# Kernel optimization log

Measured on AMD Instinct MI355X. Metric: run time of the kernel, lower is better.

## Reference

```python
import jax, jax.numpy as jnp
import numpy as np

B, T, D = 2, 2048, 1024
H, HD = 16, 64
DL, DC = 512, 256
THETA = 10000.0
LN_EPS = 1e-5


def setup_inputs() -> dict:
    key = jax.random.key(0)
    ks = jax.random.split(key, 8)
    s = 0.02
    return {
        "x": jax.random.normal(ks[0], (B, T, D), jnp.float32),
        "W_q": jax.random.normal(ks[1], (H * HD, D), jnp.float32) * s,
        "b_q": jnp.zeros((H * HD,), jnp.float32),
        "W_kvl": jax.random.normal(ks[2], (DL, D), jnp.float32) * s,
        "b_kvl": jnp.zeros((DL,), jnp.float32),
        "ts_scale": jnp.ones((DL,), jnp.float32),
        "ts_shift": jnp.zeros((DL,), jnp.float32),
        "W_comp": jax.random.normal(ks[3], (DC, DL), jnp.float32) * s,
        "W_exp": jax.random.normal(ks[4], (DL, DC), jnp.float32) * s,
        "ln_g": jnp.ones((DC,), jnp.float32),
        "ln_b": jnp.zeros((DC,), jnp.float32),
        "W_fkv": jax.random.normal(ks[5], (2 * H * HD, DL), jnp.float32) * s,
        "b_fkv": jnp.zeros((2 * H * HD,), jnp.float32),
        "W_out": jax.random.normal(ks[6], (D, H * HD), jnp.float32) * s,
        "b_out": jnp.zeros((D,), jnp.float32),
    }


def _rope_tables(t_len):
    inv_freq = 1.0 / (THETA ** (jnp.arange(0, HD, 2, dtype=jnp.float32) / HD))
    pos = jnp.arange(t_len, dtype=jnp.float32)
    freqs = pos[:, None] * inv_freq[None, :]          # [T, HD/2]
    cos = jnp.concatenate([jnp.cos(freqs)] * 2, -1)   # [T, HD]
    sin = jnp.concatenate([jnp.sin(freqs)] * 2, -1)
    return cos[None, None], sin[None, None]           # [1,1,T,HD]


def _rotate_half(z):
    return jnp.concatenate([-z[..., HD // 2:], z[..., :HD // 2]], -1)


def reference(x, W_q, b_q, W_kvl, b_kvl, ts_scale, ts_shift, W_comp, W_exp,
              ln_g, ln_b, W_fkv, b_fkv, W_out, b_out):
    # Q path: [B,T,D] -> [B,H,T,HD]
    q = (jnp.einsum('btd,ed->bte', x, W_q) + b_q).reshape(B, T, H, HD).transpose(0, 2, 1, 3)

    # KV latent + learned KVSplice bottleneck
    kvl = jnp.einsum('btd,ld->btl', x, W_kvl) + b_kvl                 # [B,T,DL]
    xt = kvl * jax.nn.softplus(ts_scale) + ts_shift
    c = jnp.einsum('btl,cl->btc', xt, W_comp)                         # [B,T,DC]
    mu = jnp.mean(c, -1, keepdims=True)
    var = jnp.mean(jnp.square(c - mu), -1, keepdims=True)
    c = (c - mu) * jax.lax.rsqrt(var + LN_EPS) * ln_g + ln_b
    dec = jnp.einsum('btc,lc->btl', c, W_exp)                         # [B,T,DL]

    # Decompress latent to K,V
    kv = jnp.einsum('btl,el->bte', dec, W_fkv) + b_fkv                # [B,T,2*H*HD]
    kv = kv.reshape(B, T, 2, H, HD).transpose(2, 0, 3, 1, 4)          # [2,B,H,T,HD]
    k, v = kv[0], kv[1]

    # RoPE
    cos, sin = _rope_tables(T)
    q = q * cos + _rotate_half(q) * sin
    k = k * cos + _rotate_half(k) * sin

    # Causal SDPA
    scale = 1.0 / np.sqrt(HD)
    scores = jnp.einsum('bhqd,bhkd->bhqk', q, k) * scale
    mask = jnp.tril(jnp.ones((T, T), bool))
    scores = jnp.where(mask, scores, jnp.float32(-1e30))
    attn = jax.nn.softmax(scores, axis=-1)
    o = jnp.einsum('bhqk,bhkd->bhqd', attn, v)
    o = o.transpose(0, 2, 1, 3).reshape(B, T, H * HD)
    return jnp.einsum('bte,de->btd', o, W_out) + b_out
```

## Files before the change

kernel.cpp:

```cpp
#include <hip/hip_runtime.h>
#include <math.h>

#define B_SZ   2
#define T_SEQ  2048
#define NH     16
#define HDIM   64
#define D_MOD  1024
#define DL     512
#define DC     256
#define MROWS  4096

typedef __attribute__((ext_vector_type(8))) short bf16x8;
typedef __attribute__((ext_vector_type(4))) float f32x4;

#define SCALE_Q 0.18033688011112042f

static __device__ __forceinline__ unsigned short f2bf(float f) {
    union { float f; unsigned u; } v; v.f = f;
    unsigned r = v.u + 0x7fffu + ((v.u >> 16) & 1u);
    return (unsigned short)(r >> 16);
}

static __device__ __forceinline__ void gl_lds16(const unsigned short* g,
                                                unsigned short* l) {
    __builtin_amdgcn_global_load_lds(
        (const __attribute__((address_space(1))) unsigned int*)g,
        (__attribute__((address_space(3))) unsigned int*)l, 16, 0, 0);
}

__global__ __launch_bounds__(256) void cvt_bf16(
    const float* __restrict__ x,  const float* __restrict__ wq,
    const float* __restrict__ wkvl, const float* __restrict__ wcomp,
    const float* __restrict__ wexp, const float* __restrict__ wfkv,
    const float* __restrict__ wout,
    unsigned short* __restrict__ xb,  unsigned short* __restrict__ wqh,
    unsigned short* __restrict__ wkvlh, unsigned short* __restrict__ wcomph,
    unsigned short* __restrict__ wexph, unsigned short* __restrict__ wfkvh,
    unsigned short* __restrict__ wouth, float2* __restrict__ rope_tab)
{
    const int g = blockIdx.x * 256 + threadIdx.x;
    const int stride = gridDim.x * 256;
#define CVT_SEG(src, dst, n4)                                              \
    for (int i = g; i < (n4); i += stride) {                               \
        float4 v = ((const float4*)(src))[i];                              \
        unsigned short h[4] = {f2bf(v.x), f2bf(v.y), f2bf(v.z), f2bf(v.w)};\
        *(uint2*)((dst) + (size_t)i * 4) = *(uint2*)h;                     \
    }
    CVT_SEG(x, xb, 1048576)
    CVT_SEG(wq, wqh, 262144)
    CVT_SEG(wkvl, wkvlh, 131072)
    CVT_SEG(wcomp, wcomph, 32768)
    CVT_SEG(wexp, wexph, 32768)
    CVT_SEG(wfkv, wfkvh, 262144)
    CVT_SEG(wout, wouth, 262144)
#undef CVT_SEG
    for (int i = g; i < T_SEQ * 32; i += stride) {
        const int t = i >> 5, fi = i & 31;
        const float inv = __expf((float)fi * (-9.210340371976184f / 32.0f));
        float sn, cs; sincosf((float)t * inv, &sn, &cs);
        rope_tab[i] = make_float2(cs, sn);
    }
}

#define GEMM64R_PROLOG(Aptr, Wptr, Kdim)                                       \
    __shared__ unsigned short As[64 * 64];                                     \
    __shared__ unsigned short Ws[64 * 64];                                     \
    const int tid = threadIdx.x;                                               \
    const int w = tid >> 6, lane = tid & 63;                                   \
    const int l16 = lane & 15, quad = lane >> 4;                               \
    const int sw8 = ((lane & 7) ^ ((lane >> 3) & 7)) << 3;                     \
    const int srow = lane >> 3;                                                \
    const unsigned short* Ag0 = (Aptr) + (size_t)(m0 + w * 16 + srow) * (Kdim) + sw8;      \
    const unsigned short* Ag1 = (Aptr) + (size_t)(m0 + w * 16 + 8 + srow) * (Kdim) + sw8;  \
    const unsigned short* Wg0 = (Wptr) + (size_t)(n0 + w * 16 + srow) * (Kdim) + sw8;      \
    const unsigned short* Wg1 = (Wptr) + (size_t)(n0 + w * 16 + 8 + srow) * (Kdim) + sw8;  \
    unsigned short* Al0 = &As[(w * 16) * 64];                                  \
    unsigned short* Al1 = &As[(w * 16 + 8) * 64];                              \
    unsigned short* Wl0 = &Ws[(w * 16) * 64];                                  \
    unsigned short* Wl1 = &Ws[(w * 16 + 8) * 64];                              \
    const int xh = (l16 & 7);                                                  \
    f32x4 acc[4];                                                              \
    _Pragma("unroll") for (int j = 0; j < 4; ++j)                              \
        acc[j] = (f32x4){0.f, 0.f, 0.f, 0.f};                                  \
    for (int k0 = 0; k0 < (Kdim); k0 += 64) {                                  \
        __syncthreads();                                                       \
        gl_lds16(Ag0 + k0, Al0);                                               \
        gl_lds16(Ag1 + k0, Al1);                                               \
        gl_lds16(Wg0 + k0, Wl0);                                               \
        gl_lds16(Wg1 + k0, Wl1);                                               \
        __syncthreads();                                                       \
        bf16x8 af[2], bfr[4][2];                                               \
        _Pragma("unroll") for (int kk = 0; kk < 2; ++kk)                       \
            af[kk] = *(const bf16x8*)&As[(w * 16 + l16) * 64 +                 \
                                         (((kk * 4 + quad) ^ xh) << 3)];       \
        _Pragma("unroll") for (int j = 0; j < 4; ++j)                          \
            _Pragma("unroll") for (int kk = 0; kk < 2; ++kk)                   \
                bfr[j][kk] = *(const bf16x8*)&Ws[(j * 16 + l16) * 64 +         \
                                             (((kk * 4 + quad) ^ xh) << 3)];   \
        _Pragma("unroll") for (int kk = 0; kk < 2; ++kk)                       \
            _Pragma("unroll") for (int j = 0; j < 4; ++j)                      \
                acc[j] = __builtin_amdgcn_mfma_f32_16x16x32_bf16(              \
                    af[kk], bfr[j][kk], acc[j], 0, 0, 0);                      \
    }

__global__ __launch_bounds__(256) void gemm_qxt(
    const unsigned short* __restrict__ A, const unsigned short* __restrict__ Wq,
    const unsigned short* __restrict__ Wkvl,
    const float* __restrict__ b_q, const float* __restrict__ b_kvl,
    const float* __restrict__ ts_scale, const float* __restrict__ ts_shift,
    const float2* __restrict__ tab,
    unsigned short* __restrict__ qh, unsigned short* __restrict__ xt)
{
    const int m0 = blockIdx.x * 64;
    const bool is_q = (blockIdx.y < 16);
    const int n0 = is_q ? blockIdx.y * 64 : (blockIdx.y - 16) * 64;
    const unsigned short* W = is_q ? Wq : Wkvl;

    GEMM64R_PROLOG(A, W, D_MOD)

    if (is_q) {
#pragma unroll
        for (int j = 0; j < 4; ++j) {
            const int col = n0 + j * 16 + l16;
            const int h = col >> 6, hd = col & 63;
            const float bv = b_q[col];
            const float bvp = b_q[col ^ 32];
            const float sgn = (hd < 32) ? -1.f : 1.f;
#pragma unroll
            for (int reg = 0; reg < 4; ++reg) {
                const int row = m0 + w * 16 + quad * 4 + reg;
                const int b = row >> 11, t = row & (T_SEQ - 1);
                const float2 cssn = tab[t * 32 + (hd & 31)];
                const float v  = acc[j][reg] + bv;
                const float vp = acc[j ^ 2][reg] + bvp;
                const float r = (v * cssn.x + sgn * vp * cssn.y) * SCALE_Q;
                qh[(((size_t)b * NH + h) * T_SEQ + t) * HDIM + hd] = f2bf(r);
            }
        }
    } else {
#pragma unroll
        for (int j = 0; j < 4; ++j) {
            const int col = n0 + j * 16 + l16;
            const float bv = b_kvl[col];
            const float sp_s = log1pf(expf(ts_scale[col]));
            const float sp_t = ts_shift[col];
#pragma unroll
            for (int reg = 0; reg < 4; ++reg) {
                const int row = m0 + w * 16 + quad * 4 + reg;
                const float val = (acc[j][reg] + bv) * sp_s + sp_t;
                xt[(size_t)row * DL + col] = f2bf(val);
            }
        }
    }
}

__global__ __launch_bounds__(256) void gemm_kv(
    const unsigned short* __restrict__ A, const unsigned short* __restrict__ W,
    const float* __restrict__ bias, const float2* __restrict__ tab,
    unsigned short* __restrict__ kh, unsigned short* __restrict__ vth)
{
    const int m0 = blockIdx.x * 64, n0 = blockIdx.y * 64;

    GEMM64R_PROLOG(A, W, DL)

    if (n0 < 1024) {
#pragma unroll
        for (int j = 0; j < 4; ++j) {
            const int col = n0 + j * 16 + l16;
            const int h = (col >> 6) & 15, hd = col & 63;
            const float bv = bias[col];
            const float bvp = bias[col ^ 32];
            const float sgn = (hd < 32) ? -1.f : 1.f;
#pragma unroll
            for (int reg = 0; reg < 4; ++reg) {
                const int row = m0 + w * 16 + quad * 4 + reg;
                const int b = row >> 11, t = row & (T_SEQ - 1);
                const float2 cssn = tab[t * 32 + (hd & 31)];
                const float v  = acc[j][reg] + bv;
                const float vp = acc[j ^ 2][reg] + bvp;
                const float r = v * cssn.x + sgn * vp * cssn.y;
                kh[(((size_t)b * NH + h) * T_SEQ + t) * HDIM + hd] = f2bf(r);
            }
        }
    } else {
#pragma unroll
        for (int j = 0; j < 4; ++j) {
            const int col = n0 + j * 16 + l16;
            const int cv = col - 1024;
            const int h = cv >> 6, hd = cv & 63;
            const float bv = bias[col];
            unsigned short hv[4];
            const int r0 = m0 + w * 16 + quad * 4;
            const int b = r0 >> 11, t0 = r0 & (T_SEQ - 1);
#pragma unroll
            for (int reg = 0; reg < 4; ++reg)
                hv[reg] = f2bf(acc[j][reg] + bv);
            *(uint2*)&vth[(((size_t)b * NH + h) * HDIM + hd) * T_SEQ + t0] =
                *(uint2*)hv;
        }
    }
}

__global__ __launch_bounds__(256) void gemm_out(
    const unsigned short* __restrict__ A, const unsigned short* __restrict__ W,
    const float* __restrict__ bias, float* __restrict__ C)
{
    const int m0 = blockIdx.x * 64, n0 = blockIdx.y * 64;

    GEMM64R_PROLOG(A, W, D_MOD)

#pragma unroll
    for (int j = 0; j < 4; ++j) {
        const int col = n0 + j * 16 + l16;
        const float bv = bias[col];
#pragma unroll
        for (int reg = 0; reg < 4; ++reg) {
            const int row = m0 + w * 16 + quad * 4 + reg;
            C[(size_t)row * D_MOD + col] = acc[j][reg] + bv;
        }
    }
}

__global__ __launch_bounds__(256) void gemm_b(
    const unsigned short* __restrict__ A, const unsigned short* __restrict__ W,
    unsigned short* __restrict__ dec)
{
    const int m0 = blockIdx.x * 64, n0 = blockIdx.y * 64;

    GEMM64R_PROLOG(A, W, DC)

#pragma unroll
    for (int j = 0; j < 4; ++j) {
        const int col = n0 + j * 16 + l16;
#pragma unroll
        for (int reg = 0; reg < 4; ++reg) {
            const int row = m0 + w * 16 + quad * 4 + reg;
            dec[(size_t)row * DL + col] = f2bf(acc[j][reg]);
        }
    }
}

__global__ __launch_bounds__(256) void gemm_c_ln(
    const unsigned short* __restrict__ A, const unsigned short* __restrict__ W,
    const float* __restrict__ g, const float* __restrict__ bta,
    unsigned short* __restrict__ outb)
{
    __shared__ unsigned short As[16 * 32];
    __shared__ unsigned short Ws[256 * 32];
    __shared__ float redS[4][16];
    __shared__ float redQ[4][16];

    const int tid = threadIdx.x;
    const int w = tid >> 6, lane = tid & 63;
    const int l16 = lane & 15, quad = lane >> 4;
    const int m0 = blockIdx.x * 16;

    const int srow = lane >> 2, scol = (lane & 3) << 3;
    const unsigned short* Ag = A + (size_t)(m0 + srow) * DL + scol;
    const unsigned short* Wg = W + (size_t)(w * 64 + srow) * DL + scol;

    f32x4 acc[4];
#pragma unroll
    for (int j = 0; j < 4; ++j) acc[j] = (f32x4){0.f, 0.f, 0.f, 0.f};

    for (int k0 = 0; k0 < DL; k0 += 32) {
        __syncthreads();
        if (w == 0) gl_lds16(Ag + k0, &As[0]);
#pragma unroll
        for (int c = 0; c < 4; ++c)
            gl_lds16(Wg + (size_t)(c * 16) * DL + k0, &Ws[(w * 64 + c * 16) * 32]);
        __syncthreads();

        const bf16x8 af = *(const bf16x8*)&As[l16 * 32 + quad * 8];
        bf16x8 bfr[4];
#pragma unroll
        for (int j = 0; j < 4; ++j)
            bfr[j] = *(const bf16x8*)&Ws[(w * 64 + j * 16 + l16) * 32 + quad * 8];
#pragma unroll
        for (int j = 0; j < 4; ++j)
            acc[j] = __builtin_amdgcn_mfma_f32_16x16x32_bf16(af, bfr[j], acc[j], 0, 0, 0);
    }

    float s[4], q2[4];
#pragma unroll
    for (int reg = 0; reg < 4; ++reg) {
        float sv = (acc[0][reg] + acc[1][reg]) + (acc[2][reg] + acc[3][reg]);
        float qv = (acc[0][reg] * acc[0][reg] + acc[1][reg] * acc[1][reg]) +
                   (acc[2][reg] * acc[2][reg] + acc[3][reg] * acc[3][reg]);
#pragma unroll
        for (int off = 1; off < 16; off <<= 1) {
            sv += __shfl_xor(sv, off);
            qv += __shfl_xor(qv, off);
        }
        s[reg] = sv; q2[reg] = qv;
    }
    if (l16 == 0) {
#pragma unroll
        for (int reg = 0; reg < 4; ++reg) {
            redS[w][quad * 4 + reg] = s[reg];
            redQ[w][quad * 4 + reg] = q2[reg];
        }
    }
    __syncthreads();

#pragma unroll
    for (int reg = 0; reg < 4; ++reg) {
        const int r = quad * 4 + reg;
        const float sum = (redS[0][r] + redS[1][r]) + (redS[2][r] + redS[3][r]);
        const float sq  = (redQ[0][r] + redQ[1][r]) + (redQ[2][r] + redQ[3][r]);
        const float mu  = sum * (1.0f / DC);
        const float var = sq * (1.0f / DC) - mu * mu;
        const float rstd = rsqrtf(var + 1e-5f);
#pragma unroll
        for (int j = 0; j < 4; ++j) {
            const int col = w * 64 + j * 16 + l16;
            const float val = (acc[j][reg] - mu) * rstd * g[col] + bta[col];
            outb[(size_t)(m0 + r) * DC + col] = f2bf(val);
        }
    }
}

__global__ __launch_bounds__(256, 3) void flash_mfma(
    const unsigned short* __restrict__ q, const unsigned short* __restrict__ k,
    const unsigned short* __restrict__ vt, unsigned short* __restrict__ o)
{
    __shared__ unsigned short Ks[64 * 72];
    __shared__ unsigned short Vs[64 * 72];
    __shared__ unsigned short Ps[64 * 72];

    const int bh = blockIdx.x & 31;
    const int j  = 31 - (blockIdx.x >> 5);
    const int q0 = j * 64;
    const int tid = threadIdx.x;
    const int w = tid >> 6, lane = tid & 63;
    const int l16 = lane & 15, quad = lane >> 4;
    const int rbase = q0 + w * 16;

    bf16x8 qf[2];
#pragma unroll
    for (int kk = 0; kk < 2; ++kk)
        qf[kk] = *(const bf16x8*)(q + ((size_t)bh * T_SEQ + rbase + l16) * HDIM + kk * 32 + quad * 8);

    f32x4 of[4];
    float lrow[4];
#pragma unroll
    for (int dt = 0; dt < 4; ++dt) of[dt] = (f32x4){0.f, 0.f, 0.f, 0.f};
#pragma unroll
    for (int r = 0; r < 4; ++r) lrow[r] = 0.f;

    const int ldr = tid >> 2;
    const int ldc = (tid & 3) * 16;
    const unsigned short* kgb = k + ((size_t)bh * T_SEQ + ldr) * HDIM + ldc;
    const unsigned short* vgb = vt + ((size_t)bh * HDIM + ldr) * T_SEQ + ldc;

    const int kend = (j + 1) * 64;
    for (int k0 = 0; k0 < kend; k0 += 64) {
        __syncthreads();
        {
            const unsigned short* kg = kgb + (size_t)k0 * HDIM;
            *(bf16x8*)&Ks[ldr * 72 + ldc]     = *(const bf16x8*)kg;
            *(bf16x8*)&Ks[ldr * 72 + ldc + 8] = *(const bf16x8*)(kg + 8);
            const unsigned short* vg = vgb + k0;
            *(bf16x8*)&Vs[ldr * 72 + ldc]     = *(const bf16x8*)vg;
            *(bf16x8*)&Vs[ldr * 72 + ldc + 8] = *(const bf16x8*)(vg + 8);
        }
        __syncthreads();

        bf16x8 kf[4][2];
#pragma unroll
        for (int nt = 0; nt < 4; ++nt)
#pragma unroll
            for (int kk = 0; kk < 2; ++kk)
                kf[nt][kk] = *(const bf16x8*)&Ks[(nt * 16 + l16) * 72 + kk * 32 + quad * 8];

        f32x4 sf[4];
#pragma unroll
        for (int nt = 0; nt < 4; ++nt) {
            sf[nt] = (f32x4){0.f, 0.f, 0.f, 0.f};
#pragma unroll
            for (int kk = 0; kk < 2; ++kk)
                sf[nt] = __builtin_amdgcn_mfma_f32_16x16x32_bf16(qf[kk], kf[nt][kk], sf[nt], 0, 0, 0);
        }

        const bool need_mask = (k0 + 63) > rbase;
#pragma unroll
        for (int reg = 0; reg < 4; ++reg) {
            float a0 = sf[0][reg], a1 = sf[1][reg], a2 = sf[2][reg], a3 = sf[3][reg];
            if (need_mask) {
                const int tq = rbase + quad * 4 + reg;
                if (k0 +      l16 > tq) a0 = -1e30f;
                if (k0 + 16 + l16 > tq) a1 = -1e30f;
                if (k0 + 32 + l16 > tq) a2 = -1e30f;
                if (k0 + 48 + l16 > tq) a3 = -1e30f;
            }
            union { float f; unsigned u; } u0, u1, u2, u3;
            u0.f = exp2f(a0); u1.f = exp2f(a1);
            u2.f = exp2f(a2); u3.f = exp2f(a3);
            const int prow = (w * 16 + quad * 4 + reg) * 72 + l16;
            Ps[prow]      = (unsigned short)(u0.u >> 16);
            Ps[prow + 16] = (unsigned short)(u1.u >> 16);
            Ps[prow + 32] = (unsigned short)(u2.u >> 16);
            Ps[prow + 48] = (unsigned short)(u3.u >> 16);
            u0.u &= 0xffff0000u; u1.u &= 0xffff0000u;
            u2.u &= 0xffff0000u; u3.u &= 0xffff0000u;
            lrow[reg] += (u0.f + u1.f) + (u2.f + u3.f);
        }

        bf16x8 vf[4][2];
#pragma unroll
        for (int dt = 0; dt < 4; ++dt)
#pragma unroll
            for (int kk = 0; kk < 2; ++kk)
                vf[dt][kk] = *(const bf16x8*)&Vs[(dt * 16 + l16) * 72 + kk * 32 + quad * 8];

        bf16x8 pf[2];
#pragma unroll
        for (int kk = 0; kk < 2; ++kk)
            pf[kk] = *(const bf16x8*)&Ps[(w * 16 + l16) * 72 + kk * 32 + quad * 8];
#pragma unroll
        for (int dt = 0; dt < 4; ++dt)
#pragma unroll
            for (int kk = 0; kk < 2; ++kk)
                of[dt] = __builtin_amdgcn_mfma_f32_16x16x32_bf16(pf[kk], vf[dt][kk], of[dt], 0, 0, 0);
    }

    const int b = bh >> 4, h = bh & 15;
#pragma unroll
    for (int reg = 0; reg < 4; ++reg) {
        float l = lrow[reg];
        l += __shfl_xor(l, 1);
        l += __shfl_xor(l, 2);
        l += __shfl_xor(l, 4);
        l += __shfl_xor(l, 8);
        const float inv = 1.0f / l;
        const int t = rbase + quad * 4 + reg;
#pragma unroll
        for (int dt = 0; dt < 4; ++dt)
            o[((size_t)b * T_SEQ + t) * (NH * HDIM) + h * HDIM + dt * 16 + l16] =
                f2bf(of[dt][reg] * inv);
    }
}

extern "C" void kernel_launch(void* const* d_in, const int* in_sizes, int n_in,
                              void* d_out, int out_size, void* d_ws, size_t ws_size,
                              hipStream_t stream)
{
    (void)in_sizes; (void)n_in; (void)out_size; (void)ws_size;

    const float* x        = (const float*)d_in[0];
    const float* W_q      = (const float*)d_in[1];
    const float* b_q      = (const float*)d_in[2];
    const float* W_kvl    = (const float*)d_in[3];
    const float* b_kvl    = (const float*)d_in[4];
    const float* ts_scale = (const float*)d_in[5];
    const float* ts_shift = (const float*)d_in[6];
    const float* W_comp   = (const float*)d_in[7];
    const float* W_exp    = (const float*)d_in[8];
    const float* ln_g     = (const float*)d_in[9];
    const float* ln_b     = (const float*)d_in[10];
    const float* W_fkv    = (const float*)d_in[11];
    const float* b_fkv    = (const float*)d_in[12];
    const float* W_out    = (const float*)d_in[13];
    const float* b_out    = (const float*)d_in[14];
    float* out = (float*)d_out;

    char* p = (char*)d_ws;
    unsigned short* xb     = (unsigned short*)p;             p += 8  * 1024 * 1024;
    unsigned short* wqh    = (unsigned short*)p;             p += 2  * 1024 * 1024;
    unsigned short* wkvlh  = (unsigned short*)p;             p += 1  * 1024 * 1024;
    unsigned short* wcomph = (unsigned short*)p;             p += 256 * 1024;
    unsigned short* wexph  = (unsigned short*)p;             p += 256 * 1024;
    unsigned short* wfkvh  = (unsigned short*)p;             p += 2  * 1024 * 1024;
    unsigned short* wouth  = (unsigned short*)p;             p += 2  * 1024 * 1024;
    unsigned short* qh     = (unsigned short*)p;             p += 8  * 1024 * 1024;
    unsigned short* kh     = (unsigned short*)p;             p += 8  * 1024 * 1024;
    unsigned short* vth    = (unsigned short*)p;             p += 8  * 1024 * 1024;
    unsigned short* xt     = (unsigned short*)p;             p += 4  * 1024 * 1024;
    unsigned short* cbh    = (unsigned short*)p;             p += 2  * 1024 * 1024;
    unsigned short* dec    = (unsigned short*)p;             p += 4  * 1024 * 1024;
    unsigned short* ob     = (unsigned short*)p;             p += 8  * 1024 * 1024;
    float2*         tab    = (float2*)p;                     p += 512 * 1024;

    const dim3 blk(256);

    cvt_bf16<<<1024, blk, 0, stream>>>(x, W_q, W_kvl, W_comp, W_exp, W_fkv, W_out,
                                       xb, wqh, wkvlh, wcomph, wexph, wfkvh, wouth,
                                       tab);

    gemm_qxt<<<dim3(64, 24), blk, 0, stream>>>(
        xb, wqh, wkvlh, b_q, b_kvl, ts_scale, ts_shift, tab, qh, xt);

    gemm_c_ln<<<256, blk, 0, stream>>>(
        xt, wcomph, ln_g, ln_b, cbh);

    gemm_b<<<dim3(64, 8), blk, 0, stream>>>(
        cbh, wexph, dec);

    gemm_kv<<<dim3(64, 32), blk, 0, stream>>>(
        dec, wfkvh, b_fkv, tab, kh, vth);

    flash_mfma<<<1024, blk, 0, stream>>>(qh, kh, vth, ob);

    gemm_out<<<dim3(64, 16), blk, 0, stream>>>(
        ob, wouth, b_out, out);
}
```

Before: 223.1 us.

## Use 128x128 block tiles with 2x2 warp layout for large GEMMs

Replaces the 64x64 block-tile GEMM core used by the Q/latent, K/V and output projections with a 128x128 tile in which each of four waves computes a 64x64 sub-tile (4x4 MFMA accumulators). Each LDS fragment load is now reused across four MFMAs instead of fewer, which raises arithmetic intensity and cuts global and LDS traffic per flop. The trade-off is a quarter as many blocks (e.g. 256–512 per launch on a 256-CU part), higher register use (64 accumulator floats per lane) and possibly lower occupancy or tail imbalance.

```diff
diff --git a/kernel.cpp b/kernel.cpp
--- a/kernel.cpp
+++ b/kernel.cpp
@@ -59,6 +59,179 @@
         const float inv = __expf((float)fi * (-9.210340371976184f / 32.0f));
         float sn, cs; sincosf((float)t * inv, &sn, &cs);
         rope_tab[i] = make_float2(cs, sn);
+    }
+}
+
+#define GEMM128_PROLOG(Aptr, Wptr, Kdim)                                       \
+    __shared__ unsigned short As[128 * 64];                                    \
+    __shared__ unsigned short Ws[128 * 64];                                    \
+    const int tid = threadIdx.x;                                               \
+    const int w = tid >> 6, lane = tid & 63;                                   \
+    const int l16 = lane & 15, quad = lane >> 4;                               \
+    const int wr = w >> 1, wc = w & 1;                                         \
+    const int srow = lane >> 3;                                                \
+    const int sw8 = ((lane & 7) ^ srow) << 3;                                  \
+    const unsigned short* Ag = (Aptr) + (size_t)(m0 + w * 32 + srow) * (Kdim) + sw8; \
+    const unsigned short* Wg = (Wptr) + (size_t)(n0 + w * 32 + srow) * (Kdim) + sw8; \
+    unsigned short* Al = &As[(w * 32) * 64];                                   \
+    unsigned short* Wl = &Ws[(w * 32) * 64];                                   \
+    const int xh = l16 & 7;                                                    \
+    f32x4 acc[4][4];                                                           \
+    _Pragma("unroll") for (int mi = 0; mi < 4; ++mi)                           \
+        _Pragma("unroll") for (int nj = 0; nj < 4; ++nj)                       \
+            acc[mi][nj] = (f32x4){0.f, 0.f, 0.f, 0.f};                         \
+    for (int k0 = 0; k0 < (Kdim); k0 += 64) {                                  \
+        __syncthreads();                                                       \
+        _Pragma("unroll") for (int seg = 0; seg < 4; ++seg) {                  \
+            gl_lds16(Ag + (size_t)(seg * 8) * (Kdim) + k0, Al + seg * 512);    \
+            gl_lds16(Wg + (size_t)(seg * 8) * (Kdim) + k0, Wl + seg * 512);    \
+        }                                                                      \
+        __syncthreads();                                                       \
+        _Pragma("unroll") for (int kk = 0; kk < 2; ++kk) {                     \
+            bf16x8 af[4], bfr[4];                                              \
+            _Pragma("unroll") for (int mi = 0; mi < 4; ++mi)                   \
+                af[mi] = *(const bf16x8*)&As[(wr * 64 + mi * 16 + l16) * 64 +  \
+                                             (((kk * 4 + quad) ^ xh) << 3)];   \
+            _Pragma("unroll") for (int nj = 0; nj < 4; ++nj)                   \
+                bfr[nj] = *(const bf16x8*)&Ws[(wc * 64 + nj * 16 + l16) * 64 + \
+                                              (((kk * 4 + quad) ^ xh) << 3)];  \
+            _Pragma("unroll") for (int mi = 0; mi < 4; ++mi)                   \
+                _Pragma("unroll") for (int nj = 0; nj < 4; ++nj)               \
+                    acc[mi][nj] = __builtin_amdgcn_mfma_f32_16x16x32_bf16(     \
+                        af[mi], bfr[nj], acc[mi][nj], 0, 0, 0);                \
+        }                                                                      \
+    }
+
+__global__ __launch_bounds__(256) void gemm_qxt(
+    const unsigned short* __restrict__ A, const unsigned short* __restrict__ Wq,
+    const unsigned short* __restrict__ Wkvl,
+    const float* __restrict__ b_q, const float* __restrict__ b_kvl,
+    const float* __restrict__ ts_scale, const float* __restrict__ ts_shift,
+    const float2* __restrict__ tab,
+    unsigned short* __restrict__ qh, unsigned short* __restrict__ xt)
+{
+    const int m0 = blockIdx.x * 128;
+    const bool is_q = (blockIdx.y < 8);
+    const int n0 = is_q ? blockIdx.y * 128 : (blockIdx.y - 8) * 128;
+    const unsigned short* W = is_q ? Wq : Wkvl;
+
+    GEMM128_PROLOG(A, W, D_MOD)
+
+    if (is_q) {
+#pragma unroll
+        for (int nj = 0; nj < 4; ++nj) {
+            const int col = n0 + wc * 64 + nj * 16 + l16;
+            const int h = col >> 6, hd = col & 63;
+            const float bv = b_q[col];
+            const float bvp = b_q[col ^ 32];
+            const float sgn = (hd < 32) ? -1.f : 1.f;
+#pragma unroll
+            for (int mi = 0; mi < 4; ++mi) {
+#pragma unroll
+                for (int reg = 0; reg < 4; ++reg) {
+                    const int row = m0 + wr * 64 + mi * 16 + quad * 4 + reg;
+                    const int b = row >> 11, t = row & (T_SEQ - 1);
+                    const float2 cssn = tab[t * 32 + (hd & 31)];
+                    const float v  = acc[mi][nj][reg] + bv;
+                    const float vp = acc[mi][nj ^ 2][reg] + bvp;
+                    const float r = (v * cssn.x + sgn * vp * cssn.y) * SCALE_Q;
+                    qh[(((size_t)b * NH + h) * T_SEQ + t) * HDIM + hd] = f2bf(r);
+                }
+            }
+        }
+    } else {
+#pragma unroll
+        for (int nj = 0; nj < 4; ++nj) {
+            const int col = n0 + wc * 64 + nj * 16 + l16;
+            const float bv = b_kvl[col];
+            const float sp_s = log1pf(expf(ts_scale[col]));
+            const float sp_t = ts_shift[col];
+#pragma unroll
+            for (int mi = 0; mi < 4; ++mi) {
+#pragma unroll
+                for (int reg = 0; reg < 4; ++reg) {
+                    const int row = m0 + wr * 64 + mi * 16 + quad * 4 + reg;
+                    const float val = (acc[mi][nj][reg] + bv) * sp_s + sp_t;
+                    xt[(size_t)row * DL + col] = f2bf(val);
+                }
+            }
+        }
+    }
+}
+
+__global__ __launch_bounds__(256) void gemm_kv(
+    const unsigned short* __restrict__ A, const unsigned short* __restrict__ W,
+    const float* __restrict__ bias, const float2* __restrict__ tab,
+    unsigned short* __restrict__ kh, unsigned short* __restrict__ vth)
+{
+    const int m0 = blockIdx.x * 128, n0 = blockIdx.y * 128;
+
+    GEMM128_PROLOG(A, W, DL)
+
+    if (n0 < 1024) {
+#pragma unroll
+        for (int nj = 0; nj < 4; ++nj) {
+            const int col = n0 + wc * 64 + nj * 16 + l16;
+            const int h = (col >> 6) & 15, hd = col & 63;
+            const float bv = bias[col];
+            const float bvp = bias[col ^ 32];
+            const float sgn = (hd < 32) ? -1.f : 1.f;
+#pragma unroll
+            for (int mi = 0; mi < 4; ++mi) {
+#pragma unroll
+                for (int reg = 0; reg < 4; ++reg) {
+                    const int row = m0 + wr * 64 + mi * 16 + quad * 4 + reg;
+                    const int b = row >> 11, t = row & (T_SEQ - 1);
+                    const float2 cssn = tab[t * 32 + (hd & 31)];
+                    const float v  = acc[mi][nj][reg] + bv;
+                    const float vp = acc[mi][nj ^ 2][reg] + bvp;
+                    const float r = v * cssn.x + sgn * vp * cssn.y;
+                    kh[(((size_t)b * NH + h) * T_SEQ + t) * HDIM + hd] = f2bf(r);
+                }
+            }
+        }
+    } else {
+#pragma unroll
+        for (int nj = 0; nj < 4; ++nj) {
+            const int col = n0 + wc * 64 + nj * 16 + l16;
+            const int cv = col - 1024;
+            const int h = cv >> 6, hd = cv & 63;
+            const float bv = bias[col];
+#pragma unroll
+            for (int mi = 0; mi < 4; ++mi) {
+                unsigned short hv[4];
+                const int r0 = m0 + wr * 64 + mi * 16 + quad * 4;
+                const int b = r0 >> 11, t0 = r0 & (T_SEQ - 1);
+#pragma unroll
+                for (int reg = 0; reg < 4; ++reg)
+                    hv[reg] = f2bf(acc[mi][nj][reg] + bv);
+                *(uint2*)&vth[(((size_t)b * NH + h) * HDIM + hd) * T_SEQ + t0] =
+                    *(uint2*)hv;
+            }
+        }
+    }
+}
+
+__global__ __launch_bounds__(256) void gemm_out(
+    const unsigned short* __restrict__ A, const unsigned short* __restrict__ W,
+    const float* __restrict__ bias, float* __restrict__ C)
+{
+    const int m0 = blockIdx.x * 128, n0 = blockIdx.y * 128;
+
+    GEMM128_PROLOG(A, W, D_MOD)
+
+#pragma unroll
+    for (int nj = 0; nj < 4; ++nj) {
+        const int col = n0 + wc * 64 + nj * 16 + l16;
+        const float bv = bias[col];
+#pragma unroll
+        for (int mi = 0; mi < 4; ++mi) {
+#pragma unroll
+            for (int reg = 0; reg < 4; ++reg) {
+                const int row = m0 + wr * 64 + mi * 16 + quad * 4 + reg;
+                C[(size_t)row * D_MOD + col] = acc[mi][nj][reg] + bv;
+            }
+        }
     }
 }
 
@@ -103,124 +276,6 @@
                     af[kk], bfr[j][kk], acc[j], 0, 0, 0);                      \
     }
 
-__global__ __launch_bounds__(256) void gemm_qxt(
-    const unsigned short* __restrict__ A, const unsigned short* __restrict__ Wq,
-    const unsigned short* __restrict__ Wkvl,
-    const float* __restrict__ b_q, const float* __restrict__ b_kvl,
-    const float* __restrict__ ts_scale, const float* __restrict__ ts_shift,
-    const float2* __restrict__ tab,
-    unsigned short* __restrict__ qh, unsigned short* __restrict__ xt)
-{
-    const int m0 = blockIdx.x * 64;
-    const bool is_q = (blockIdx.y < 16);
-    const int n0 = is_q ? blockIdx.y * 64 : (blockIdx.y - 16) * 64;
-    const unsigned short* W = is_q ? Wq : Wkvl;
-
-    GEMM64R_PROLOG(A, W, D_MOD)
-
-    if (is_q) {
-#pragma unroll
-        for (int j = 0; j < 4; ++j) {
-            const int col = n0 + j * 16 + l16;
-            const int h = col >> 6, hd = col & 63;
-            const float bv = b_q[col];
-            const float bvp = b_q[col ^ 32];
-            const float sgn = (hd < 32) ? -1.f : 1.f;
-#pragma unroll
-            for (int reg = 0; reg < 4; ++reg) {
-                const int row = m0 + w * 16 + quad * 4 + reg;
-                const int b = row >> 11, t = row & (T_SEQ - 1);
-                const float2 cssn = tab[t * 32 + (hd & 31)];
-                const float v  = acc[j][reg] + bv;
-                const float vp = acc[j ^ 2][reg] + bvp;
-                const float r = (v * cssn.x + sgn * vp * cssn.y) * SCALE_Q;
-                qh[(((size_t)b * NH + h) * T_SEQ + t) * HDIM + hd] = f2bf(r);
-            }
-        }
-    } else {
-#pragma unroll
-        for (int j = 0; j < 4; ++j) {
-            const int col = n0 + j * 16 + l16;
-            const float bv = b_kvl[col];
-            const float sp_s = log1pf(expf(ts_scale[col]));
-            const float sp_t = ts_shift[col];
-#pragma unroll
-            for (int reg = 0; reg < 4; ++reg) {
-                const int row = m0 + w * 16 + quad * 4 + reg;
-                const float val = (acc[j][reg] + bv) * sp_s + sp_t;
-                xt[(size_t)row * DL + col] = f2bf(val);
-            }
-        }
-    }
-}
-
-__global__ __launch_bounds__(256) void gemm_kv(
-    const unsigned short* __restrict__ A, const unsigned short* __restrict__ W,
-    const float* __restrict__ bias, const float2* __restrict__ tab,
-    unsigned short* __restrict__ kh, unsigned short* __restrict__ vth)
-{
-    const int m0 = blockIdx.x * 64, n0 = blockIdx.y * 64;
-
-    GEMM64R_PROLOG(A, W, DL)
-
-    if (n0 < 1024) {
-#pragma unroll
-        for (int j = 0; j < 4; ++j) {
-            const int col = n0 + j * 16 + l16;
-            const int h = (col >> 6) & 15, hd = col & 63;
-            const float bv = bias[col];
-            const float bvp = bias[col ^ 32];
-            const float sgn = (hd < 32) ? -1.f : 1.f;
-#pragma unroll
-            for (int reg = 0; reg < 4; ++reg) {
-                const int row = m0 + w * 16 + quad * 4 + reg;
-                const int b = row >> 11, t = row & (T_SEQ - 1);
-                const float2 cssn = tab[t * 32 + (hd & 31)];
-                const float v  = acc[j][reg] + bv;
-                const float vp = acc[j ^ 2][reg] + bvp;
-                const float r = v * cssn.x + sgn * vp * cssn.y;
-                kh[(((size_t)b * NH + h) * T_SEQ + t) * HDIM + hd] = f2bf(r);
-            }
-        }
-    } else {
-#pragma unroll
-        for (int j = 0; j < 4; ++j) {
-            const int col = n0 + j * 16 + l16;
-            const int cv = col - 1024;
-            const int h = cv >> 6, hd = cv & 63;
-            const float bv = bias[col];
-            unsigned short hv[4];
-            const int r0 = m0 + w * 16 + quad * 4;
-            const int b = r0 >> 11, t0 = r0 & (T_SEQ - 1);
-#pragma unroll
-            for (int reg = 0; reg < 4; ++reg)
-                hv[reg] = f2bf(acc[j][reg] + bv);
-            *(uint2*)&vth[(((size_t)b * NH + h) * HDIM + hd) * T_SEQ + t0] =
-                *(uint2*)hv;
-        }
-    }
-}
-
-__global__ __launch_bounds__(256) void gemm_out(
-    const unsigned short* __restrict__ A, const unsigned short* __restrict__ W,
-    const float* __restrict__ bias, float* __restrict__ C)
-{
-    const int m0 = blockIdx.x * 64, n0 = blockIdx.y * 64;
-
-    GEMM64R_PROLOG(A, W, D_MOD)
-
-#pragma unroll
-    for (int j = 0; j < 4; ++j) {
-        const int col = n0 + j * 16 + l16;
-        const float bv = bias[col];
-#pragma unroll
-        for (int reg = 0; reg < 4; ++reg) {
-            const int row = m0 + w * 16 + quad * 4 + reg;
-            C[(size_t)row * D_MOD + col] = acc[j][reg] + bv;
-        }
-    }
-}
-
 __global__ __launch_bounds__(256) void gemm_b(
     const unsigned short* __restrict__ A, const unsigned short* __restrict__ W,
     unsigned short* __restrict__ dec)
@@ -487,7 +542,7 @@
                                        xb, wqh, wkvlh, wcomph, wexph, wfkvh, wouth,
                                        tab);
 
-    gemm_qxt<<<dim3(64, 24), blk, 0, stream>>>(
+    gemm_qxt<<<dim3(32, 12), blk, 0, stream>>>(
         xb, wqh, wkvlh, b_q, b_kvl, ts_scale, ts_shift, tab, qh, xt);
 
     gemm_c_ln<<<256, blk, 0, stream>>>(
@@ -496,11 +551,11 @@
     gemm_b<<<dim3(64, 8), blk, 0, stream>>>(
         cbh, wexph, dec);
 
-    gemm_kv<<<dim3(64, 32), blk, 0, stream>>>(
+    gemm_kv<<<dim3(32, 16), blk, 0, stream>>>(
         dec, wfkvh, b_fkv, tab, kh, vth);
 
     flash_mfma<<<1024, blk, 0, stream>>>(qh, kh, vth, ob);
 
-    gemm_out<<<dim3(64, 16), blk, 0, stream>>>(
+    gemm_out<<<dim3(32, 8), blk, 0, stream>>>(
         ob, wouth, b_out, out);
 }
```

Result: slower. 244.9 us (+9.8%).

## Double-buffer K/V tiles with register prefetch and raise MFMA wave priority

Applied to the files above, without the earlier changes.

The flash attention loop now loads the next K and V tile from global memory into registers while the current tile is being computed. It stores the tiles into two alternating LDS buffers, which removes one of the two barriers per iteration. It also wraps both MFMA blocks in s_setprio so waves issuing matrix instructions get scheduling priority. The cost is double the K/V LDS footprint and extra registers, which could reduce occupancy at the declared launch bounds.

```diff
diff --git a/kernel.cpp b/kernel.cpp
--- a/kernel.cpp
+++ b/kernel.cpp
@@ -324,8 +324,8 @@
     const unsigned short* __restrict__ q, const unsigned short* __restrict__ k,
     const unsigned short* __restrict__ vt, unsigned short* __restrict__ o)
 {
-    __shared__ unsigned short Ks[64 * 72];
-    __shared__ unsigned short Vs[64 * 72];
+    __shared__ unsigned short Ks[2][64 * 72];
+    __shared__ unsigned short Vs[2][64 * 72];
     __shared__ unsigned short Ps[64 * 72];
 
     const int bh = blockIdx.x & 31;
@@ -353,27 +353,37 @@
     const unsigned short* kgb = k + ((size_t)bh * T_SEQ + ldr) * HDIM + ldc;
     const unsigned short* vgb = vt + ((size_t)bh * HDIM + ldr) * T_SEQ + ldc;
 
+    bf16x8 kr0 = *(const bf16x8*)kgb;
+    bf16x8 kr1 = *(const bf16x8*)(kgb + 8);
+    bf16x8 vr0 = *(const bf16x8*)vgb;
+    bf16x8 vr1 = *(const bf16x8*)(vgb + 8);
+
     const int kend = (j + 1) * 64;
-    for (int k0 = 0; k0 < kend; k0 += 64) {
+    int buf = 0;
+    for (int k0 = 0; k0 < kend; k0 += 64, buf ^= 1) {
+        *(bf16x8*)&Ks[buf][ldr * 72 + ldc]     = kr0;
+        *(bf16x8*)&Ks[buf][ldr * 72 + ldc + 8] = kr1;
+        *(bf16x8*)&Vs[buf][ldr * 72 + ldc]     = vr0;
+        *(bf16x8*)&Vs[buf][ldr * 72 + ldc + 8] = vr1;
+        if (k0 + 64 < kend) {
+            const unsigned short* kg = kgb + (size_t)(k0 + 64) * HDIM;
+            const unsigned short* vg = vgb + (k0 + 64);
+            kr0 = *(const bf16x8*)kg;
+            kr1 = *(const bf16x8*)(kg + 8);
+            vr0 = *(const bf16x8*)vg;
+            vr1 = *(const bf16x8*)(vg + 8);
+        }
         __syncthreads();
-        {
-            const unsigned short* kg = kgb + (size_t)k0 * HDIM;
-            *(bf16x8*)&Ks[ldr * 72 + ldc]     = *(const bf16x8*)kg;
-            *(bf16x8*)&Ks[ldr * 72 + ldc + 8] = *(const bf16x8*)(kg + 8);
-            const unsigned short* vg = vgb + k0;
-            *(bf16x8*)&Vs[ldr * 72 + ldc]     = *(const bf16x8*)vg;
-            *(bf16x8*)&Vs[ldr * 72 + ldc + 8] = *(const bf16x8*)(vg + 8);
-        }
-        __syncthreads();
 
         bf16x8 kf[4][2];
 #pragma unroll
         for (int nt = 0; nt < 4; ++nt)
 #pragma unroll
             for (int kk = 0; kk < 2; ++kk)
-                kf[nt][kk] = *(const bf16x8*)&Ks[(nt * 16 + l16) * 72 + kk * 32 + quad * 8];
+                kf[nt][kk] = *(const bf16x8*)&Ks[buf][(nt * 16 + l16) * 72 + kk * 32 + quad * 8];
 
         f32x4 sf[4];
+        __builtin_amdgcn_s_setprio(1);
 #pragma unroll
         for (int nt = 0; nt < 4; ++nt) {
             sf[nt] = (f32x4){0.f, 0.f, 0.f, 0.f};
@@ -381,6 +391,7 @@
             for (int kk = 0; kk < 2; ++kk)
                 sf[nt] = __builtin_amdgcn_mfma_f32_16x16x32_bf16(qf[kk], kf[nt][kk], sf[nt], 0, 0, 0);
         }
+        __builtin_amdgcn_s_setprio(0);
 
         const bool need_mask = (k0 + 63) > rbase;
 #pragma unroll
@@ -411,17 +422,19 @@
         for (int dt = 0; dt < 4; ++dt)
 #pragma unroll
             for (int kk = 0; kk < 2; ++kk)
-                vf[dt][kk] = *(const bf16x8*)&Vs[(dt * 16 + l16) * 72 + kk * 32 + quad * 8];
+                vf[dt][kk] = *(const bf16x8*)&Vs[buf][(dt * 16 + l16) * 72 + kk * 32 + quad * 8];
 
         bf16x8 pf[2];
 #pragma unroll
         for (int kk = 0; kk < 2; ++kk)
             pf[kk] = *(const bf16x8*)&Ps[(w * 16 + l16) * 72 + kk * 32 + quad * 8];
+        __builtin_amdgcn_s_setprio(1);
 #pragma unroll
         for (int dt = 0; dt < 4; ++dt)
 #pragma unroll
             for (int kk = 0; kk < 2; ++kk)
                 of[dt] = __builtin_amdgcn_mfma_f32_16x16x32_bf16(pf[kk], vf[dt][kk], of[dt], 0, 0, 0);
+        __builtin_amdgcn_s_setprio(0);
     }
 
     const int b = bh >> 4, h = bh & 15;
```

Result: faster. 218.4 us (-2.1%).
